# Kernel tuning notes

Measured on AMD Instinct MI355X. Metric: run time of the kernel, lower is better.

The kernel has to match this reference:

```python
import jax, jax.numpy as jnp
import numpy as np

B, N, CIN, COUT, K, E = 2048, 64, 128, 256, 3, 256
EPS = 1e-5


def setup_inputs() -> dict:
    key = jax.random.key(0)
    ks = jax.random.split(key, 8)
    x = jax.random.normal(ks[0], (B, N, CIN), dtype=jnp.float32)
    edge_index = jax.random.randint(ks[1], (2, E), 0, N, dtype=jnp.int32)
    W = jax.random.normal(ks[2], (CIN, COUT), dtype=jnp.float32) / np.sqrt(CIN)
    b_gcn = jnp.zeros((COUT,), jnp.float32)
    w_conv = jax.random.normal(ks[3], (COUT, COUT, K), dtype=jnp.float32) / np.sqrt(COUT * K)
    b_conv = jnp.zeros((COUT,), jnp.float32)
    gamma = jnp.ones((COUT,), jnp.float32)
    beta = jnp.zeros((COUT,), jnp.float32)
    return {"x": x, "W": W, "b_gcn": b_gcn, "w_conv": w_conv, "b_conv": b_conv,
            "gamma": gamma, "beta": beta, "edge_index": edge_index}


def reference(x, W, b_gcn, w_conv, b_conv, gamma, beta, edge_index):
    Bq, Nn, _ = x.shape
    Co = W.shape[1]
    # ---- GCNConv (PyG semantics: xW, add self-loops, symmetric norm, + bias) ----
    src, dst = edge_index[0], edge_index[1]
    loop = jnp.arange(Nn, dtype=edge_index.dtype)
    src2 = jnp.concatenate([src, loop])           # [E+N]
    dst2 = jnp.concatenate([dst, loop])
    deg = jnp.zeros((Nn,), x.dtype).at[dst2].add(1.0)
    dinv = jnp.where(deg > 0, jax.lax.rsqrt(deg), 0.0)
    norm = dinv[src2] * dinv[dst2]                # [E+N]
    xw = jnp.einsum('bnc,co->bno', x, W)          # [B, N, Co]
    msgs = xw[:, src2, :] * norm[None, :, None]   # [B, E+N, Co]
    x_gcn = jnp.zeros((Bq, Nn, Co), x.dtype).at[:, dst2, :].add(msgs) + b_gcn
    # ---- temporal Conv1d over batch_seq axis, shared weights across nodes ----
    xt = x_gcn.transpose(1, 2, 0)                 # [N, Co, B]  (time = batch_seq)
    pad = K // 2
    y = jax.lax.conv_general_dilated(xt, w_conv, (1,), [(pad, pad)],
                                     dimension_numbers=('NCH', 'OIH', 'NCH'))
    y = y + b_conv[None, :, None]                 # [N, Co, B]
    # ---- BatchNorm1d (training-mode batch stats) + ReLU ----
    y = y.transpose(2, 1, 0)                      # [B, Co, N]
    mean = y.mean(axis=(0, 2), keepdims=True)
    var = ((y - mean) ** 2).mean(axis=(0, 2), keepdims=True)
    y = (y - mean) * jax.lax.rsqrt(var + EPS)
    y = gamma[None, :, None] * y + beta[None, :, None]
    y = jax.nn.relu(y)
    # dropout is identity in eval mode
    return y.transpose(0, 2, 1)                   # [B, N, Co]
```

## Files before the change

### kernel.cpp

```cpp
#include <hip/hip_runtime.h>
#include <hip/hip_bf16.h>

typedef __attribute__((ext_vector_type(8))) unsigned short us8;
typedef __attribute__((ext_vector_type(4))) unsigned short us4;
typedef __attribute__((ext_vector_type(8))) short short8;
typedef __attribute__((ext_vector_type(4))) float f32x4;

#define BB 2048
#define NN 64
#define CIN 128
#define CO 256
#define KWIN 3
#define EE 256
#define NE 320
#define EPSBN 1e-5f

static __device__ __forceinline__ void gload_lds16(const unsigned short* g, unsigned short* l) {
    __builtin_amdgcn_global_load_lds(
        (const __attribute__((address_space(1))) unsigned int*)g,
        (__attribute__((address_space(3))) unsigned int*)l,
        16, 0, 0);
}

static __device__ __forceinline__ float bf2f(unsigned short u) {
    return __uint_as_float(((unsigned int)u) << 16);
}

static __device__ __forceinline__ unsigned short f2bfu(float f) {
    unsigned int u = __float_as_uint(f);
    u = (u + 0x7FFFu + ((u >> 16) & 1u)) >> 16;
    return (unsigned short)u;
}

__global__ __launch_bounds__(320) void k_setup(const int* __restrict__ ei,
                                               __hip_bfloat16* __restrict__ Ahat) {
    __shared__ int s_cnt[NN * NN];
    __shared__ int s_deg[NN];
    __shared__ float s_dinv[NN];
    const int t = threadIdx.x;
    for (int i = t; i < NN * NN; i += 320) s_cnt[i] = 0;
    if (t < NN) s_deg[t] = 0;
    __syncthreads();
    int src, dst;
    if (t < EE) { src = ei[t]; dst = ei[EE + t]; }
    else        { src = t - EE; dst = t - EE; }
    atomicAdd(&s_deg[dst], 1);
    atomicAdd(&s_cnt[dst * NN + src], 1);
    __syncthreads();
    if (t < NN) s_dinv[t] = rsqrtf((float)s_deg[t]);
    __syncthreads();
    for (int i = t; i < NN * NN; i += 320) {
        const int n = i >> 6, m = i & 63;
        Ahat[i] = __float2bfloat16((float)s_cnt[i] * s_dinv[m] * s_dinv[n]);
    }
}

__global__ __launch_bounds__(256) void k_weights(const float* __restrict__ W,
                                                 const float* __restrict__ wconv,
                                                 __hip_bfloat16* __restrict__ Wt,
                                                 __hip_bfloat16* __restrict__ W2f) {
    const int idx = blockIdx.x * 256 + threadIdx.x;
    if (idx < CO * CIN) {
        const int o = idx >> 7, c = idx & 127;
        Wt[idx] = __float2bfloat16(W[c * CO + o]);
    }
    const int j = idx - CO * CIN;
    if (j >= 0 && j < CO * KWIN * CO) {
        const int o16 = j / 12288, r = j - o16 * 12288;
        const int kc = r >> 9, r2 = r & 511;
        const int l = r2 >> 3, e = r2 & 7;
        const int o = o16 * 16 + (l & 15);
        const int k = kc * 32 + (l >> 4) * 8 + e;
        W2f[j] = __float2bfloat16(wconv[(o * CO + (k & 255)) * KWIN + (k >> 8)]);
    }
}

__global__ __launch_bounds__(256) void k_gcn(const float* __restrict__ x,
                                             const __hip_bfloat16* __restrict__ Ahat_,
                                             const __hip_bfloat16* __restrict__ Wt_,
                                             const float* __restrict__ bgcn,
                                             __hip_bfloat16* __restrict__ xgcn_) {
    __shared__ __align__(16) unsigned short sx[64 * 128];
    __shared__ __align__(16) unsigned short stm[256 * 64];
    const unsigned short* Ahat = (const unsigned short*)Ahat_;
    const unsigned short* Wt   = (const unsigned short*)Wt_;
    unsigned short* xgcn = (unsigned short*)xgcn_;

    const int b = blockIdx.x, tid = threadIdx.x;
    const int lane = tid & 63, wid = tid >> 6;
    const int llo = lane & 15, lhi = lane >> 4;

#pragma unroll
    for (int r = 0; r < 4; ++r) {
        const int f = tid + 256 * r;
        const int m = f >> 4, c0 = (f & 15) * 8;
        const float4* src = (const float4*)(x + ((size_t)b * NN + m) * CIN + c0);
        const float4 v0 = src[0], v1 = src[1];
        unsigned short t8[8] = {f2bfu(v0.x), f2bfu(v0.y), f2bfu(v0.z), f2bfu(v0.w),
                                f2bfu(v1.x), f2bfu(v1.y), f2bfu(v1.z), f2bfu(v1.w)};
        *(us8*)&sx[m * 128 + (c0 ^ ((m & 7) << 3))] = *(const us8*)t8;
    }
    __syncthreads();

    f32x4 acc1[4][4];
#pragma unroll
    for (int p = 0; p < 4; ++p)
#pragma unroll
        for (int q = 0; q < 4; ++q) acc1[p][q] = (f32x4){0.f, 0.f, 0.f, 0.f};
#pragma unroll
    for (int s = 0; s < 4; ++s) {
        const int k0 = s * 32 + lhi * 8;
        short8 af[4], bf[4];
#pragma unroll
        for (int p = 0; p < 4; ++p) {
            const int m = p * 16 + llo;
            af[p] = *(const short8*)&sx[m * 128 + (k0 ^ ((m & 7) << 3))];
        }
#pragma unroll
        for (int q = 0; q < 4; ++q) {
            const int o = wid * 64 + q * 16 + llo;
            bf[q] = *(const short8*)&Wt[o * 128 + k0];
        }
#pragma unroll
        for (int p = 0; p < 4; ++p)
#pragma unroll
            for (int q = 0; q < 4; ++q)
                acc1[p][q] = __builtin_amdgcn_mfma_f32_16x16x32_bf16(af[p], bf[q], acc1[p][q], 0, 0, 0);
    }
#pragma unroll
    for (int p = 0; p < 4; ++p)
#pragma unroll
        for (int q = 0; q < 4; ++q) {
            const int o = wid * 64 + q * 16 + llo;
            const int bm = p * 16 + lhi * 4;
            unsigned short t4[4] = {f2bfu(acc1[p][q][0]), f2bfu(acc1[p][q][1]),
                                    f2bfu(acc1[p][q][2]), f2bfu(acc1[p][q][3])};
            *(us4*)&stm[o * 64 + (bm ^ ((o & 7) << 3))] = *(const us4*)t4;
        }

    f32x4 acc2[4][4];
#pragma unroll
    for (int p = 0; p < 4; ++p)
#pragma unroll
        for (int q = 0; q < 4; ++q) acc2[p][q] = (f32x4){0.f, 0.f, 0.f, 0.f};
#pragma unroll
    for (int s = 0; s < 2; ++s) {
        const int k0 = s * 32 + lhi * 8;
        short8 af[4], bf[4];
#pragma unroll
        for (int p = 0; p < 4; ++p) {
            const int n = p * 16 + llo;
            af[p] = *(const short8*)&Ahat[n * 64 + k0];
        }
#pragma unroll
        for (int q = 0; q < 4; ++q) {
            const int o = wid * 64 + q * 16 + llo;
            bf[q] = *(const short8*)&stm[o * 64 + (k0 ^ ((o & 7) << 3))];
        }
#pragma unroll
        for (int p = 0; p < 4; ++p)
#pragma unroll
            for (int q = 0; q < 4; ++q)
                acc2[p][q] = __builtin_amdgcn_mfma_f32_16x16x32_bf16(af[p], bf[q], acc2[p][q], 0, 0, 0);
    }

    float bg[4];
#pragma unroll
    for (int q = 0; q < 4; ++q) bg[q] = bgcn[wid * 64 + q * 16 + llo];
#pragma unroll
    for (int p = 0; p < 4; ++p)
#pragma unroll
        for (int q = 0; q < 4; ++q) {
            const int o = wid * 64 + q * 16 + llo;
#pragma unroll
            for (int reg = 0; reg < 4; ++reg) {
                const int n = p * 16 + lhi * 4 + reg;
                xgcn[((size_t)n * BB + b) * CO + o] = f2bfu(acc2[p][q][reg] + bg[q]);
            }
        }
}

__global__ __launch_bounds__(512, 4) void k_conv(const __hip_bfloat16* __restrict__ xgcn_,
                                                 const __hip_bfloat16* __restrict__ W2f_,
                                                 const float* __restrict__ bconv,
                                                 __hip_bfloat16* __restrict__ y_,
                                                 float* __restrict__ partials) {
    __shared__ __align__(16) unsigned short sA[130 * 256];
    const unsigned short* xgcn = (const unsigned short*)xgcn_;
    const unsigned short* W2f  = (const unsigned short*)W2f_;
    unsigned short* y = (unsigned short*)y_;

    const int tt = blockIdx.x, n = blockIdx.y;
    const int tid = threadIdx.x;
    const int lane = tid & 63, wid = tid >> 6;
    const int t0 = tt * 128;
    const int wm0 = (wid >> 2) * 64;
    const int wo0 = (wid & 3) * 64;
    const int lhi = lane >> 4, llo = lane & 15;

    f32x4 acc[4][4];
#pragma unroll
    for (int m = 0; m < 4; ++m)
#pragma unroll
        for (int q = 0; q < 4; ++q) acc[m][q] = (f32x4){0.f, 0.f, 0.f, 0.f};

    {
        const int rsub = lane >> 5;
        const int g = lane & 31;
        for (int iss = wid; iss < 65; iss += 8) {
            const int r = 2 * iss + rsub;
            int bg = t0 - 1 + r;
            bg = min(max(bg, 0), BB - 1);
            const int col = ((g ^ (r & 7)) << 3);
            gload_lds16(xgcn + ((size_t)n * BB + bg) * CO + col, sA + iss * 512);
        }
    }
    __syncthreads();
    if (tt == 0 || tt == 15) {
        const int zr = (tt == 0) ? 0 : 129;
        if (tid < 32) *(uint4*)&sA[zr * 256 + tid * 8] = make_uint4(0u, 0u, 0u, 0u);
        __syncthreads();
    }

    const unsigned short* bq[4];
#pragma unroll
    for (int q = 0; q < 4; ++q) {
        const int o16 = (wid & 3) * 4 + q;
        bq[q] = W2f + ((size_t)o16 * 24) * 512 + lane * 8;
    }
#pragma unroll 4
    for (int kc = 0; kc < 24; ++kc) {
        const int kk = kc >> 3;
        const int G = (kc & 7) * 4 + lhi;
        short8 af[4], bf[4];
#pragma unroll
        for (int m = 0; m < 4; ++m) {
            const int sr = wm0 + m * 16 + llo + kk;
            af[m] = *(const short8*)&sA[sr * 256 + ((G ^ (sr & 7)) << 3)];
        }
#pragma unroll
        for (int q = 0; q < 4; ++q)
            bf[q] = *(const short8*)(bq[q] + kc * 512);
#pragma unroll
        for (int m = 0; m < 4; ++m)
#pragma unroll
            for (int q = 0; q < 4; ++q)
                acc[m][q] = __builtin_amdgcn_mfma_f32_16x16x32_bf16(af[m], bf[q], acc[m][q], 0, 0, 0);
    }

    float bc[4], s1v[4], s2v[4];
#pragma unroll
    for (int q = 0; q < 4; ++q) {
        bc[q] = bconv[wo0 + q * 16 + llo];
        s1v[q] = 0.f; s2v[q] = 0.f;
    }
#pragma unroll
    for (int m = 0; m < 4; ++m) {
#pragma unroll
        for (int reg = 0; reg < 4; ++reg) {
            const int trow = t0 + wm0 + m * 16 + lhi * 4 + reg;
            unsigned short* dst = y + ((size_t)trow * NN + n) * CO + wo0 + llo;
#pragma unroll
            for (int q = 0; q < 4; ++q) {
                const float v = acc[m][q][reg] + bc[q];
                dst[q * 16] = f2bfu(v);
                s1v[q] += v;
                s2v[q] += v * v;
            }
        }
    }
    __syncthreads();
    float* sred1 = (float*)sA;
    float* sred2 = sred1 + 2048;
    const int rg = (wid >> 2) * 4 + lhi;
#pragma unroll
    for (int q = 0; q < 4; ++q) {
        const int cl = wo0 + q * 16 + llo;
        sred1[rg * 256 + cl] = s1v[q];
        sred2[rg * 256 + cl] = s2v[q];
    }
    __syncthreads();
    if (tid < 256) {
        float a = 0.f, b2 = 0.f;
#pragma unroll
        for (int r = 0; r < 8; ++r) { a += sred1[r * 256 + tid]; b2 += sred2[r * 256 + tid]; }
        float* pb = partials + (size_t)(n * 16 + tt) * 512;
        pb[tid * 2]     = a;
        pb[tid * 2 + 1] = b2;
    }
}

__global__ __launch_bounds__(256) void k_bnstats(const float* __restrict__ partials,
                                                 const float* __restrict__ gamma,
                                                 const float* __restrict__ beta,
                                                 float* __restrict__ scl,
                                                 float* __restrict__ shf) {
    const int o = blockIdx.x, tid = threadIdx.x;
    float s1 = 0.f, s2 = 0.f;
    for (int i = tid; i < 1024; i += 256) {
        const float* p = partials + (size_t)i * 512 + o * 2;
        s1 += p[0]; s2 += p[1];
    }
    __shared__ float r1[256], r2[256];
    r1[tid] = s1; r2[tid] = s2;
    __syncthreads();
    for (int s = 128; s > 0; s >>= 1) {
        if (tid < s) { r1[tid] += r1[tid + s]; r2[tid] += r2[tid + s]; }
        __syncthreads();
    }
    if (tid == 0) {
        const float inv = 1.f / (float)((size_t)BB * NN);
        const float mean = r1[0] * inv;
        const float var  = r2[0] * inv - mean * mean;
        const float sc = gamma[o] * rsqrtf(var + EPSBN);
        scl[o] = sc;
        shf[o] = beta[o] - mean * sc;
    }
}

__global__ __launch_bounds__(256) void k_apply(const unsigned short* __restrict__ y,
                                               float* __restrict__ out,
                                               const float* __restrict__ scl,
                                               const float* __restrict__ shf) {
    __shared__ float ssc[CO], ssh[CO];
    const int tid = threadIdx.x;
    ssc[tid] = scl[tid]; ssh[tid] = shf[tid];
    __syncthreads();
    const size_t total8 = (size_t)BB * NN * CO / 8;
    float4* out4 = (float4*)out;
    for (size_t i = (size_t)blockIdx.x * 256 + tid; i < total8; i += (size_t)gridDim.x * 256) {
        const us8 v = *(const us8*)(y + i * 8);
        const int ob = (int)((i * 8) & (CO - 1));
        float4 r0, r1;
        r0.x = fmaxf(0.f, bf2f(v[0]) * ssc[ob + 0] + ssh[ob + 0]);
        r0.y = fmaxf(0.f, bf2f(v[1]) * ssc[ob + 1] + ssh[ob + 1]);
        r0.z = fmaxf(0.f, bf2f(v[2]) * ssc[ob + 2] + ssh[ob + 2]);
        r0.w = fmaxf(0.f, bf2f(v[3]) * ssc[ob + 3] + ssh[ob + 3]);
        r1.x = fmaxf(0.f, bf2f(v[4]) * ssc[ob + 4] + ssh[ob + 4]);
        r1.y = fmaxf(0.f, bf2f(v[5]) * ssc[ob + 5] + ssh[ob + 5]);
        r1.z = fmaxf(0.f, bf2f(v[6]) * ssc[ob + 6] + ssh[ob + 6]);
        r1.w = fmaxf(0.f, bf2f(v[7]) * ssc[ob + 7] + ssh[ob + 7]);
        out4[i * 2]     = r0;
        out4[i * 2 + 1] = r1;
    }
}

extern "C" void kernel_launch(void* const* d_in, const int* in_sizes, int n_in,
                              void* d_out, int out_size, void* d_ws, size_t ws_size,
                              hipStream_t stream) {
    const float* x     = (const float*)d_in[0];
    const float* W     = (const float*)d_in[1];
    const float* bgcn  = (const float*)d_in[2];
    const float* wconv = (const float*)d_in[3];
    const float* bconv = (const float*)d_in[4];
    const float* gamma = (const float*)d_in[5];
    const float* beta  = (const float*)d_in[6];
    const int*   ei    = (const int*)d_in[7];
    float* out = (float*)d_out;

    char* ws = (char*)d_ws;
    size_t off = 0;
    __hip_bfloat16* xgcn = (__hip_bfloat16*)(ws + off); off += (size_t)BB * NN * CO * 2;
    __hip_bfloat16* ybuf = (__hip_bfloat16*)(ws + off); off += (size_t)BB * NN * CO * 2;
    __hip_bfloat16* W2f  = (__hip_bfloat16*)(ws + off); off += (size_t)CO * KWIN * CO * 2;
    __hip_bfloat16* Ahat = (__hip_bfloat16*)(ws + off); off += (size_t)NN * NN * 2;
    __hip_bfloat16* Wt   = (__hip_bfloat16*)(ws + off); off += (size_t)CO * CIN * 2;
    float* partials = (float*)(ws + off); off += (size_t)1024 * 512 * 4;
    float* scl = (float*)(ws + off); off += 256 * 4;
    float* shf = (float*)(ws + off); off += 256 * 4;

    k_setup<<<1, 320, 0, stream>>>(ei, Ahat);
    k_weights<<<896, 256, 0, stream>>>(W, wconv, Wt, W2f);
    k_gcn<<<BB, 256, 0, stream>>>(x, Ahat, Wt, bgcn, xgcn);
    k_conv<<<dim3(16, 64), 512, 0, stream>>>(xgcn, W2f, bconv, ybuf, partials);
    k_bnstats<<<256, 256, 0, stream>>>(partials, gamma, beta, scl, shf);
    k_apply<<<2048, 256, 0, stream>>>((const unsigned short*)ybuf, out, scl, shf);
}
```

Before: 157.2 us.

## Merge setup kernels and retile conv warps to span all 128 rows

The adjacency setup and weight-conversion kernels are merged into one launch, with an extra block building Ahat, which removes a kernel launch. In the temporal conv, each of the 8 waves now covers all 128 time rows and 32 output channels instead of a 64x64 tile. B fragments come from global memory and A from LDS, so this cuts per-wave global weight loads but doubles LDS A-fragment reads. MFMA sections are also wrapped in s_setprio to raise wave priority during compute.

```diff
diff --git a/kernel.cpp b/kernel.cpp
--- a/kernel.cpp
+++ b/kernel.cpp
@@ -32,34 +32,37 @@
     return (unsigned short)u;
 }
 
-__global__ __launch_bounds__(320) void k_setup(const int* __restrict__ ei,
-                                               __hip_bfloat16* __restrict__ Ahat) {
+__global__ __launch_bounds__(256) void k_prep(const int* __restrict__ ei,
+                                              const float* __restrict__ W,
+                                              const float* __restrict__ wconv,
+                                              __hip_bfloat16* __restrict__ Ahat,
+                                              __hip_bfloat16* __restrict__ Wt,
+                                              __hip_bfloat16* __restrict__ W2f) {
     __shared__ int s_cnt[NN * NN];
     __shared__ int s_deg[NN];
     __shared__ float s_dinv[NN];
     const int t = threadIdx.x;
-    for (int i = t; i < NN * NN; i += 320) s_cnt[i] = 0;
-    if (t < NN) s_deg[t] = 0;
-    __syncthreads();
-    int src, dst;
-    if (t < EE) { src = ei[t]; dst = ei[EE + t]; }
-    else        { src = t - EE; dst = t - EE; }
-    atomicAdd(&s_deg[dst], 1);
-    atomicAdd(&s_cnt[dst * NN + src], 1);
-    __syncthreads();
-    if (t < NN) s_dinv[t] = rsqrtf((float)s_deg[t]);
-    __syncthreads();
-    for (int i = t; i < NN * NN; i += 320) {
-        const int n = i >> 6, m = i & 63;
-        Ahat[i] = __float2bfloat16((float)s_cnt[i] * s_dinv[m] * s_dinv[n]);
-    }
-}
-
-__global__ __launch_bounds__(256) void k_weights(const float* __restrict__ W,
-                                                 const float* __restrict__ wconv,
-                                                 __hip_bfloat16* __restrict__ Wt,
-                                                 __hip_bfloat16* __restrict__ W2f) {
-    const int idx = blockIdx.x * 256 + threadIdx.x;
+    if (blockIdx.x == 896) {
+        for (int i = t; i < NN * NN; i += 256) s_cnt[i] = 0;
+        if (t < NN) s_deg[t] = 0;
+        __syncthreads();
+        for (int e = t; e < NE; e += 256) {
+            int src, dst;
+            if (e < EE) { src = ei[e]; dst = ei[EE + e]; }
+            else        { src = e - EE; dst = e - EE; }
+            atomicAdd(&s_deg[dst], 1);
+            atomicAdd(&s_cnt[dst * NN + src], 1);
+        }
+        __syncthreads();
+        if (t < NN) s_dinv[t] = rsqrtf((float)s_deg[t]);
+        __syncthreads();
+        for (int i = t; i < NN * NN; i += 256) {
+            const int n = i >> 6, m = i & 63;
+            Ahat[i] = __float2bfloat16((float)s_cnt[i] * s_dinv[m] * s_dinv[n]);
+        }
+        return;
+    }
+    const int idx = blockIdx.x * 256 + t;
     if (idx < CO * CIN) {
         const int o = idx >> 7, c = idx & 127;
         Wt[idx] = __float2bfloat16(W[c * CO + o]);
@@ -194,15 +197,14 @@
     const int tid = threadIdx.x;
     const int lane = tid & 63, wid = tid >> 6;
     const int t0 = tt * 128;
-    const int wm0 = (wid >> 2) * 64;
-    const int wo0 = (wid & 3) * 64;
+    const int wo0 = wid * 32;
     const int lhi = lane >> 4, llo = lane & 15;
 
-    f32x4 acc[4][4];
-#pragma unroll
-    for (int m = 0; m < 4; ++m)
-#pragma unroll
-        for (int q = 0; q < 4; ++q) acc[m][q] = (f32x4){0.f, 0.f, 0.f, 0.f};
+    f32x4 acc[8][2];
+#pragma unroll
+    for (int p = 0; p < 8; ++p)
+#pragma unroll
+        for (int q = 0; q < 2; ++q) acc[p][q] = (f32x4){0.f, 0.f, 0.f, 0.f};
 
     {
         const int rsub = lane >> 5;
@@ -222,47 +224,49 @@
         __syncthreads();
     }
 
-    const unsigned short* bq[4];
-#pragma unroll
-    for (int q = 0; q < 4; ++q) {
-        const int o16 = (wid & 3) * 4 + q;
+    const unsigned short* bq[2];
+#pragma unroll
+    for (int q = 0; q < 2; ++q) {
+        const int o16 = wid * 2 + q;
         bq[q] = W2f + ((size_t)o16 * 24) * 512 + lane * 8;
     }
 #pragma unroll 4
     for (int kc = 0; kc < 24; ++kc) {
         const int kk = kc >> 3;
         const int G = (kc & 7) * 4 + lhi;
-        short8 af[4], bf[4];
-#pragma unroll
-        for (int m = 0; m < 4; ++m) {
-            const int sr = wm0 + m * 16 + llo + kk;
-            af[m] = *(const short8*)&sA[sr * 256 + ((G ^ (sr & 7)) << 3)];
-        }
-#pragma unroll
-        for (int q = 0; q < 4; ++q)
+        short8 af[8], bf[2];
+#pragma unroll
+        for (int p = 0; p < 8; ++p) {
+            const int sr = p * 16 + llo + kk;
+            af[p] = *(const short8*)&sA[sr * 256 + ((G ^ (sr & 7)) << 3)];
+        }
+#pragma unroll
+        for (int q = 0; q < 2; ++q)
             bf[q] = *(const short8*)(bq[q] + kc * 512);
-#pragma unroll
-        for (int m = 0; m < 4; ++m)
-#pragma unroll
-            for (int q = 0; q < 4; ++q)
-                acc[m][q] = __builtin_amdgcn_mfma_f32_16x16x32_bf16(af[m], bf[q], acc[m][q], 0, 0, 0);
-    }
-
-    float bc[4], s1v[4], s2v[4];
-#pragma unroll
-    for (int q = 0; q < 4; ++q) {
+        __builtin_amdgcn_s_setprio(1);
+#pragma unroll
+        for (int p = 0; p < 8; ++p)
+#pragma unroll
+            for (int q = 0; q < 2; ++q)
+                acc[p][q] = __builtin_amdgcn_mfma_f32_16x16x32_bf16(af[p], bf[q], acc[p][q], 0, 0, 0);
+        __builtin_amdgcn_s_setprio(0);
+    }
+
+    float bc[2], s1v[2], s2v[2];
+#pragma unroll
+    for (int q = 0; q < 2; ++q) {
         bc[q] = bconv[wo0 + q * 16 + llo];
         s1v[q] = 0.f; s2v[q] = 0.f;
     }
 #pragma unroll
-    for (int m = 0; m < 4; ++m) {
+    for (int p = 0; p < 8; ++p) {
 #pragma unroll
         for (int reg = 0; reg < 4; ++reg) {
-            const int trow = t0 + wm0 + m * 16 + lhi * 4 + reg;
+            const int trow = t0 + p * 16 + lhi * 4 + reg;
             unsigned short* dst = y + ((size_t)trow * NN + n) * CO + wo0 + llo;
 #pragma unroll
-            for (int q = 0; q < 4; ++q) {
-                const float v = acc[m][q][reg] + bc[q];
+            for (int q = 0; q < 2; ++q) {
+                const float v = acc[p][q][reg] + bc[q];
                 dst[q * 16] = f2bfu(v);
                 s1v[q] += v;
                 s2v[q] += v * v;
@@ -271,19 +275,18 @@
     }
     __syncthreads();
     float* sred1 = (float*)sA;
-    float* sred2 = sred1 + 2048;
-    const int rg = (wid >> 2) * 4 + lhi;
-#pragma unroll
-    for (int q = 0; q < 4; ++q) {
+    float* sred2 = sred1 + 1024;
+#pragma unroll
+    for (int q = 0; q < 2; ++q) {
         const int cl = wo0 + q * 16 + llo;
-        sred1[rg * 256 + cl] = s1v[q];
-        sred2[rg * 256 + cl] = s2v[q];
+        sred1[lhi * 256 + cl] = s1v[q];
+        sred2[lhi * 256 + cl] = s2v[q];
     }
     __syncthreads();
     if (tid < 256) {
         float a = 0.f, b2 = 0.f;
 #pragma unroll
-        for (int r = 0; r < 8; ++r) { a += sred1[r * 256 + tid]; b2 += sred2[r * 256 + tid]; }
+        for (int r = 0; r < 4; ++r) { a += sred1[r * 256 + tid]; b2 += sred2[r * 256 + tid]; }
         float* pb = partials + (size_t)(n * 16 + tt) * 512;
         pb[tid * 2]     = a;
         pb[tid * 2 + 1] = b2;
@@ -369,8 +372,7 @@
     float* scl = (float*)(ws + off); off += 256 * 4;
     float* shf = (float*)(ws + off); off += 256 * 4;
 
-    k_setup<<<1, 320, 0, stream>>>(ei, Ahat);
-    k_weights<<<896, 256, 0, stream>>>(W, wconv, Wt, W2f);
+    k_prep<<<897, 256, 0, stream>>>(ei, W, wconv, Ahat, Wt, W2f);
     k_gcn<<<BB, 256, 0, stream>>>(x, Ahat, Wt, bgcn, xgcn);
     k_conv<<<dim3(16, 64), 512, 0, stream>>>(xgcn, W2f, bconv, ybuf, partials);
     k_bnstats<<<256, 256, 0, stream>>>(partials, gamma, beta, scl, shf);
```

Result: faster. 148.0 us (-5.9%).
